# Kernel tuning notes

Measured on AMD Instinct MI355X. Metric: run time of the kernel, lower is better.

The kernel has to match this reference:

```python
import jax, jax.numpy as jnp
import numpy as np
import math

B, S, HID, H = 2, 1024, 768, 12
D = HID // H  # 64
ALPHA = 32.0


def setup_inputs() -> dict:
    key = jax.random.key(0)
    ks = jax.random.split(key, 8)
    return {
        "hidden_states": jax.random.normal(ks[0], (B, S, HID), jnp.float32),
        "attention_mask": jnp.zeros((B, 1, 1, S), jnp.float32),
        "head_mask": jnp.ones((1, H, 1, 1), jnp.float32),
        "rel_pos": jax.random.normal(ks[1], (B, H, S, S), jnp.float32),
        "rel_2d_pos": jax.random.normal(ks[2], (B, H, S, S), jnp.float32),
        "Wq": jax.random.normal(ks[3], (HID, HID), jnp.float32) * 0.02,
        "bq": jnp.zeros((HID,), jnp.float32),
        "Wk": jax.random.normal(ks[4], (HID, HID), jnp.float32) * 0.02,
        "bk": jnp.zeros((HID,), jnp.float32),
        "Wv": jax.random.normal(ks[5], (HID, HID), jnp.float32) * 0.02,
        "bv": jnp.zeros((HID,), jnp.float32),
    }


def _heads(x):
    # [B,S,HID] -> [B,H,S,D]
    return x.reshape(B, S, H, D).transpose(0, 2, 1, 3)


def cogview_softmax(scores, alpha=ALPHA):
    s = scores / alpha
    m = jnp.max(s, axis=-1, keepdims=True)
    return jax.nn.softmax((s - m) * alpha, axis=-1)


def reference(hidden_states, attention_mask, head_mask, rel_pos, rel_2d_pos,
              Wq, bq, Wk, bk, Wv, bv):
    norm = math.sqrt(D)
    q = _heads(hidden_states @ Wq + bq) / norm   # [B,H,S,D]
    k = _heads(hidden_states @ Wk + bk)
    v = _heads(hidden_states @ Wv + bv)
    scores = jnp.einsum("bhsd,bhtd->bhst", q, k)
    scores = scores + (rel_pos + rel_2d_pos) / norm
    scores = scores + attention_mask
    probs = cogview_softmax(scores)              # [B,H,S,S]
    probs = probs * head_mask
    ctx = jnp.einsum("bhst,bhtd->bhsd", probs, v)
    ctx = ctx.transpose(0, 2, 1, 3).reshape(B, S, HID)
    return ctx
```

## Files before the change

### kernel.cpp

```cpp
#include <hip/hip_runtime.h>
#include <hip/hip_bf16.h>
#include <cstdint>

#define BB   2
#define SS   1024
#define HIDD 768
#define NH   12
#define DH   64
#define BH   (BB*NH)

typedef short bf16x8 __attribute__((ext_vector_type(8)));
typedef float f32x4  __attribute__((ext_vector_type(4)));

__device__ __forceinline__ unsigned short f2b(float x) {
    union { float f; uint32_t u; } v; v.f = x;
    uint32_t u = v.u;
    uint32_t r = (u + 0x7fffu + ((u >> 16) & 1u)) >> 16;
    return (unsigned short)r;
}

__device__ __forceinline__ void async16(const void* g, void* l) {
    __builtin_amdgcn_global_load_lds(
        (const __attribute__((address_space(1))) unsigned int*)g,
        (__attribute__((address_space(3))) unsigned int*)l,
        16, 0, 0);
}

__global__ void cvt_x(const float* __restrict__ x, unsigned short* __restrict__ xb) {
    int i = blockIdx.x * blockDim.x + threadIdx.x;
    float4 v = ((const float4*)x)[i];
    ushort4 o;
    o.x = f2b(v.x); o.y = f2b(v.y); o.z = f2b(v.z); o.w = f2b(v.w);
    ((ushort4*)xb)[i] = o;
}

__global__ void transpose_w(const float* __restrict__ Wq, const float* __restrict__ Wk,
                            const float* __restrict__ Wv, unsigned short* __restrict__ Wt) {
    __shared__ float tile[32][33];
    const int w = blockIdx.z;
    const float* W = (w == 0) ? Wq : (w == 1) ? Wk : Wv;
    const int tx = threadIdx.x & 31, ty = threadIdx.x >> 5;
    const int k0 = blockIdx.x * 32, n0 = blockIdx.y * 32;
    for (int p = 0; p < 4; ++p)
        tile[ty + p * 8][tx] = W[(k0 + ty + p * 8) * HIDD + n0 + tx];
    __syncthreads();
    for (int p = 0; p < 4; ++p) {
        int n = n0 + ty + p * 8;
        Wt[(w * HIDD + n) * HIDD + k0 + tx] = f2b(tile[tx][ty + p * 8]);
    }
}

__global__ __launch_bounds__(256) void qkv_gemm(
    const unsigned short* __restrict__ Xb, const unsigned short* __restrict__ Wt,
    const float* __restrict__ bq, const float* __restrict__ bk, const float* __restrict__ bv,
    unsigned short* __restrict__ Qh, unsigned short* __restrict__ Kh,
    unsigned short* __restrict__ Vh) {
    __shared__ __align__(16) unsigned short lA[64 * 32];
    __shared__ __align__(16) unsigned short lB[128 * 32];
    const int t = threadIdx.x;
    const int wave = t >> 6, lane = t & 63;
    const int l15 = lane & 15, quad = lane >> 4;
    const int m0 = blockIdx.x * 64;
    const int n0 = blockIdx.y * 128;
    const int wm = (wave >> 1) * 32, wn = (wave & 1) * 64;

    f32x4 acc[2][4] = {};

    for (int k0 = 0; k0 < HIDD; k0 += 32) {
        __syncthreads();
        {
            int ldsA = (wave * 64) * 8;
            async16(Xb + (m0 + (t >> 2)) * HIDD + k0 + (t & 3) * 8, &lA[ldsA]);
            for (int r = 0; r < 2; ++r) {
                int i = r * 256 + t;
                int ldsB = (r * 256 + wave * 64) * 8;
                async16(Wt + (n0 + (i >> 2)) * HIDD + k0 + (i & 3) * 8, &lB[ldsB]);
            }
        }
        __syncthreads();

        bf16x8 af[2], bf[4];
        #pragma unroll
        for (int i = 0; i < 2; ++i)
            af[i] = *(const bf16x8*)&lA[(wm + i * 16 + l15) * 32 + quad * 8];
        #pragma unroll
        for (int j = 0; j < 4; ++j)
            bf[j] = *(const bf16x8*)&lB[(wn + j * 16 + l15) * 32 + quad * 8];
        #pragma unroll
        for (int i = 0; i < 2; ++i)
            #pragma unroll
            for (int j = 0; j < 4; ++j)
                acc[i][j] = __builtin_amdgcn_mfma_f32_16x16x32_bf16(af[i], bf[j], acc[i][j], 0, 0, 0);
    }

    const int sect = (n0 >= 1536) ? 2 : (n0 >= 768) ? 1 : 0;
    const float* bias = (sect == 0) ? bq : (sect == 1) ? bk : bv;
    unsigned short* dst = (sect == 0) ? Qh : (sect == 1) ? Kh : Vh;
    const float scale = (sect == 0) ? 0.125f : 1.0f;
    #pragma unroll
    for (int i = 0; i < 2; ++i) {
        #pragma unroll
        for (int j = 0; j < 4; ++j) {
            int n  = n0 + wn + j * 16 + l15;
            int nn = n - sect * HIDD;
            int h = nn >> 6, d = nn & 63;
            float bval = bias[nn];
            #pragma unroll
            for (int r = 0; r < 4; ++r) {
                int m = m0 + wm + i * 16 + quad * 4 + r;
                int b = m >> 10, s = m & 1023;
                float v = (acc[i][j][r] + bval) * scale;
                dst[((size_t)(b * NH + h) * SS + s) * DH + d] = f2b(v);
            }
        }
    }
}

__global__ __launch_bounds__(256) void transpose_v(
    const unsigned short* __restrict__ Vh, unsigned short* __restrict__ VhT) {
    __shared__ unsigned short tile[64][65];
    const int t = threadIdx.x;
    const int bh = blockIdx.y;
    const int s0 = blockIdx.x * 64;
    const int tx = t & 63, ty = t >> 6;
    const unsigned short* src = Vh + (size_t)bh * SS * DH;
    #pragma unroll
    for (int p = 0; p < 16; ++p)
        tile[ty + p * 4][tx] = src[(size_t)(s0 + ty + p * 4) * DH + tx];
    __syncthreads();
    unsigned short* dst = VhT + (size_t)bh * DH * SS;
    #pragma unroll
    for (int p = 0; p < 16; ++p)
        dst[(size_t)(ty + p * 4) * SS + s0 + tx] = tile[tx][ty + p * 4];
}

__global__ __launch_bounds__(256) void flash_attn(
    const unsigned short* __restrict__ Qh, const unsigned short* __restrict__ Kh,
    const unsigned short* __restrict__ VhT,
    const float* __restrict__ rel, const float* __restrict__ rel2d,
    const float* __restrict__ amask, const float* __restrict__ hmask,
    float* __restrict__ out) {
    __shared__ __align__(16) unsigned short Plds[4][16 * 72];
    __shared__ float o_lds[4][16][64];
    __shared__ float m_lds[4][16];
    __shared__ float l_lds[4][16];

    const int t = threadIdx.x;
    const int wave = t >> 6, lane = t & 63;
    const int l15 = lane & 15, quad = lane >> 4;
    const int bh = blockIdx.y;
    const int b = bh / NH, h = bh % NH;
    const int m0 = blockIdx.x * 16;

    const unsigned short* Qp = Qh + (size_t)bh * SS * DH;
    const unsigned short* Kp = Kh + (size_t)bh * SS * DH;
    const unsigned short* Vp = VhT + (size_t)bh * DH * SS;
    const float* relp  = rel   + (size_t)bh * SS * SS;
    const float* rel2p = rel2d + (size_t)bh * SS * SS;
    const float* maskp = amask + (size_t)b * SS;

    bf16x8 qf0 = *(const bf16x8*)&Qp[(m0 + l15) * DH + quad * 8];
    bf16x8 qf1 = *(const bf16x8*)&Qp[(m0 + l15) * DH + 32 + quad * 8];

    f32x4 o[4] = {};
    float mrow[4] = {-1e30f, -1e30f, -1e30f, -1e30f};
    float lrow[4] = {0.f, 0.f, 0.f, 0.f};
    unsigned short* Pw = &Plds[wave][0];

    const int jbeg = wave * 256, jend = jbeg + 256;
    for (int j0 = jbeg; j0 < jend; j0 += 64) {
        f32x4 sc[4] = {};
        #pragma unroll
        for (int c = 0; c < 4; ++c) {
            bf16x8 k0f = *(const bf16x8*)&Kp[(j0 + c * 16 + l15) * DH + quad * 8];
            bf16x8 k1f = *(const bf16x8*)&Kp[(j0 + c * 16 + l15) * DH + 32 + quad * 8];
            sc[c] = __builtin_amdgcn_mfma_f32_16x16x32_bf16(qf0, k0f, sc[c], 0, 0, 0);
            sc[c] = __builtin_amdgcn_mfma_f32_16x16x32_bf16(qf1, k1f, sc[c], 0, 0, 0);
        }
        float sv[4][4];
        #pragma unroll
        for (int c = 0; c < 4; ++c) {
            int col = j0 + c * 16 + l15;
            float mk = maskp[col];
            #pragma unroll
            for (int r = 0; r < 4; ++r) {
                size_t idx = (size_t)(m0 + quad * 4 + r) * SS + col;
                sv[c][r] = sc[c][r] + (relp[idx] + rel2p[idx]) * 0.125f + mk;
            }
        }
        float alpha[4];
        #pragma unroll
        for (int r = 0; r < 4; ++r) {
            float mx = fmaxf(fmaxf(sv[0][r], sv[1][r]), fmaxf(sv[2][r], sv[3][r]));
            #pragma unroll
            for (int off = 1; off < 16; off <<= 1) mx = fmaxf(mx, __shfl_xor(mx, off, 64));
            float mnew = fmaxf(mrow[r], mx);
            alpha[r] = __expf(mrow[r] - mnew);
            mrow[r] = mnew;
            float rs = 0.f;
            #pragma unroll
            for (int c = 0; c < 4; ++c) {
                float p = __expf(sv[c][r] - mnew);
                sv[c][r] = p;
                rs += p;
            }
            #pragma unroll
            for (int off = 1; off < 16; off <<= 1) rs += __shfl_xor(rs, off, 64);
            lrow[r] = lrow[r] * alpha[r] + rs;
            o[0][r] *= alpha[r]; o[1][r] *= alpha[r]; o[2][r] *= alpha[r]; o[3][r] *= alpha[r];
        }
        #pragma unroll
        for (int c = 0; c < 4; ++c)
            #pragma unroll
            for (int r = 0; r < 4; ++r)
                Pw[(quad * 4 + r) * 72 + c * 16 + l15] = f2b(sv[c][r]);

        bf16x8 pf0 = *(const bf16x8*)&Pw[l15 * 72 + quad * 8];
        bf16x8 pf1 = *(const bf16x8*)&Pw[l15 * 72 + 32 + quad * 8];
        #pragma unroll
        for (int dt = 0; dt < 4; ++dt) {
            bf16x8 v0 = *(const bf16x8*)&Vp[(dt * 16 + l15) * SS + j0 + quad * 8];
            bf16x8 v1 = *(const bf16x8*)&Vp[(dt * 16 + l15) * SS + j0 + 32 + quad * 8];
            o[dt] = __builtin_amdgcn_mfma_f32_16x16x32_bf16(pf0, v0, o[dt], 0, 0, 0);
            o[dt] = __builtin_amdgcn_mfma_f32_16x16x32_bf16(pf1, v1, o[dt], 0, 0, 0);
        }
    }

    #pragma unroll
    for (int dt = 0; dt < 4; ++dt)
        #pragma unroll
        for (int r = 0; r < 4; ++r)
            o_lds[wave][quad * 4 + r][dt * 16 + l15] = o[dt][r];
    if (l15 == 0) {
        #pragma unroll
        for (int r = 0; r < 4; ++r) {
            m_lds[wave][quad * 4 + r] = mrow[r];
            l_lds[wave][quad * 4 + r] = lrow[r];
        }
    }
    __syncthreads();

    const float hm = hmask[h];
    const int col = t & 63, rsel = t >> 6;
    #pragma unroll
    for (int rr = 0; rr < 4; ++rr) {
        int row = rsel * 4 + rr;
        float m01 = fmaxf(m_lds[0][row], m_lds[1][row]);
        float m23 = fmaxf(m_lds[2][row], m_lds[3][row]);
        float mt = fmaxf(m01, m23);
        float lt = 0.f, val = 0.f;
        #pragma unroll
        for (int w = 0; w < 4; ++w) {
            float sc = __expf(m_lds[w][row] - mt);
            lt += sc * l_lds[w][row];
            val += sc * o_lds[w][row][col];
        }
        int s = m0 + row;
        out[((size_t)(b * SS + s)) * HIDD + h * DH + col] = val * hm / lt;
    }
}

extern "C" void kernel_launch(void* const* d_in, const int* in_sizes, int n_in,
                              void* d_out, int out_size, void* d_ws, size_t ws_size,
                              hipStream_t stream) {
    const float* hs    = (const float*)d_in[0];
    const float* am    = (const float*)d_in[1];
    const float* hm    = (const float*)d_in[2];
    const float* rel   = (const float*)d_in[3];
    const float* rel2d = (const float*)d_in[4];
    const float* Wq    = (const float*)d_in[5];
    const float* bq    = (const float*)d_in[6];
    const float* Wk    = (const float*)d_in[7];
    const float* bk    = (const float*)d_in[8];
    const float* Wv    = (const float*)d_in[9];
    const float* bv    = (const float*)d_in[10];
    float* out = (float*)d_out;

    unsigned short* Xb  = (unsigned short*)d_ws;
    unsigned short* Wt  = Xb + 2048 * HIDD;
    unsigned short* Qh  = Wt + 3 * HIDD * HIDD;
    unsigned short* Kh  = Qh + (size_t)BH * SS * DH;
    unsigned short* Vh  = Kh + (size_t)BH * SS * DH;
    unsigned short* VhT = Vh + (size_t)BH * SS * DH;

    cvt_x<<<(2048 * HIDD / 4) / 256, 256, 0, stream>>>(hs, Xb);
    dim3 gT(24, 24, 3);
    transpose_w<<<gT, 256, 0, stream>>>(Wq, Wk, Wv, Wt);
    dim3 gG(32, 18);
    qkv_gemm<<<gG, 256, 0, stream>>>(Xb, Wt, bq, bk, bv, Qh, Kh, Vh);
    dim3 gV(16, BH);
    transpose_v<<<gV, 256, 0, stream>>>(Vh, VhT);
    dim3 gF(64, BH);
    flash_attn<<<gF, 256, 0, stream>>>(Qh, Kh, VhT, rel, rel2d, am, hm, out);
}
```

Before: 287.1 us.

## Vectorize rel-pos bias loads via LDS transpose and double-buffer QKV GEMM

In flash_attn, each lane now loads rel_pos, rel_2d_pos and the mask as float4 rows, so memory access is fully coalesced. The combined bias is then transposed through a per-wave LDS staging buffer into the MFMA accumulator layout, and that buffer is reused for the final cross-wave reduction. The QKV GEMM is retiled to 128x64 blocks with double-buffered async LDS loads, so the next k-slab is fetched while the current one is computed. The cost is extra LDS traffic for the staging step and one more barrier before the reduction.

Result: no change. 288.2 us (+0.4%).

```diff
diff --git a/kernel.cpp b/kernel.cpp
--- a/kernel.cpp
+++ b/kernel.cpp
@@ -55,37 +55,40 @@
     const float* __restrict__ bq, const float* __restrict__ bk, const float* __restrict__ bv,
     unsigned short* __restrict__ Qh, unsigned short* __restrict__ Kh,
     unsigned short* __restrict__ Vh) {
-    __shared__ __align__(16) unsigned short lA[64 * 32];
-    __shared__ __align__(16) unsigned short lB[128 * 32];
+    __shared__ __align__(16) unsigned short lA[2][128 * 32];
+    __shared__ __align__(16) unsigned short lB[2][64 * 32];
     const int t = threadIdx.x;
     const int wave = t >> 6, lane = t & 63;
     const int l15 = lane & 15, quad = lane >> 4;
-    const int m0 = blockIdx.x * 64;
-    const int n0 = blockIdx.y * 128;
-    const int wm = (wave >> 1) * 32, wn = (wave & 1) * 64;
+    const int m0 = blockIdx.x * 128;
+    const int n0 = blockIdx.y * 64;
+    const int wm = wave * 32;
 
     f32x4 acc[2][4] = {};
 
-    for (int k0 = 0; k0 < HIDD; k0 += 32) {
+    auto stage = [&](int k0, int b) {
+        #pragma unroll
+        for (int r = 0; r < 2; ++r) {
+            int ci = r * 256 + t;
+            async16(Xb + (m0 + (ci >> 2)) * HIDD + k0 + (ci & 3) * 8,
+                    &lA[b][(r * 256 + wave * 64) * 8]);
+        }
+        async16(Wt + (n0 + (t >> 2)) * HIDD + k0 + (t & 3) * 8,
+                &lB[b][(wave * 64) * 8]);
+    };
+
+    stage(0, 0);
+    for (int ki = 0; ki < 24; ++ki) {
+        const int cur = ki & 1;
         __syncthreads();
-        {
-            int ldsA = (wave * 64) * 8;
-            async16(Xb + (m0 + (t >> 2)) * HIDD + k0 + (t & 3) * 8, &lA[ldsA]);
-            for (int r = 0; r < 2; ++r) {
-                int i = r * 256 + t;
-                int ldsB = (r * 256 + wave * 64) * 8;
-                async16(Wt + (n0 + (i >> 2)) * HIDD + k0 + (i & 3) * 8, &lB[ldsB]);
-            }
-        }
-        __syncthreads();
-
+        if (ki < 23) stage((ki + 1) * 32, cur ^ 1);
         bf16x8 af[2], bf[4];
         #pragma unroll
         for (int i = 0; i < 2; ++i)
-            af[i] = *(const bf16x8*)&lA[(wm + i * 16 + l15) * 32 + quad * 8];
+            af[i] = *(const bf16x8*)&lA[cur][(wm + i * 16 + l15) * 32 + quad * 8];
         #pragma unroll
         for (int j = 0; j < 4; ++j)
-            bf[j] = *(const bf16x8*)&lB[(wn + j * 16 + l15) * 32 + quad * 8];
+            bf[j] = *(const bf16x8*)&lB[cur][(j * 16 + l15) * 32 + quad * 8];
         #pragma unroll
         for (int i = 0; i < 2; ++i)
             #pragma unroll
@@ -101,7 +104,7 @@
     for (int i = 0; i < 2; ++i) {
         #pragma unroll
         for (int j = 0; j < 4; ++j) {
-            int n  = n0 + wn + j * 16 + l15;
+            int n  = n0 + j * 16 + l15;
             int nn = n - sect * HIDD;
             int h = nn >> 6, d = nn & 63;
             float bval = bias[nn];
@@ -141,9 +144,7 @@
     const float* __restrict__ amask, const float* __restrict__ hmask,
     float* __restrict__ out) {
     __shared__ __align__(16) unsigned short Plds[4][16 * 72];
-    __shared__ float o_lds[4][16][64];
-    __shared__ float m_lds[4][16];
-    __shared__ float l_lds[4][16];
+    __shared__ __align__(16) float smem[5376];
 
     const int t = threadIdx.x;
     const int wave = t >> 6, lane = t & 63;
@@ -166,9 +167,19 @@
     float mrow[4] = {-1e30f, -1e30f, -1e30f, -1e30f};
     float lrow[4] = {0.f, 0.f, 0.f, 0.f};
     unsigned short* Pw = &Plds[wave][0];
+    float* stg = &smem[wave * 1344];
 
     const int jbeg = wave * 256, jend = jbeg + 256;
     for (int j0 = jbeg; j0 < jend; j0 += 64) {
+        f32x4 ra[4], rb[4];
+        #pragma unroll
+        for (int i = 0; i < 4; ++i) {
+            size_t base = (size_t)(m0 + 4 * i + quad) * SS + j0 + 4 * l15;
+            ra[i] = *(const f32x4*)&relp[base];
+            rb[i] = *(const f32x4*)&rel2p[base];
+        }
+        f32x4 mk4 = *(const f32x4*)&maskp[j0 + 4 * l15];
+
         f32x4 sc[4] = {};
         #pragma unroll
         for (int c = 0; c < 4; ++c) {
@@ -177,17 +188,21 @@
             sc[c] = __builtin_amdgcn_mfma_f32_16x16x32_bf16(qf0, k0f, sc[c], 0, 0, 0);
             sc[c] = __builtin_amdgcn_mfma_f32_16x16x32_bf16(qf1, k1f, sc[c], 0, 0, 0);
         }
+
+        #pragma unroll
+        for (int i = 0; i < 4; ++i)
+            #pragma unroll
+            for (int cc = 0; cc < 4; ++cc)
+                stg[(4 * l15 + cc) * 21 + 4 * i + quad] =
+                    (ra[i][cc] + rb[i][cc]) * 0.125f + mk4[cc];
+
         float sv[4][4];
         #pragma unroll
-        for (int c = 0; c < 4; ++c) {
-            int col = j0 + c * 16 + l15;
-            float mk = maskp[col];
-            #pragma unroll
-            for (int r = 0; r < 4; ++r) {
-                size_t idx = (size_t)(m0 + quad * 4 + r) * SS + col;
-                sv[c][r] = sc[c][r] + (relp[idx] + rel2p[idx]) * 0.125f + mk;
-            }
-        }
+        for (int c = 0; c < 4; ++c)
+            #pragma unroll
+            for (int r = 0; r < 4; ++r)
+                sv[c][r] = sc[c][r] + stg[(c * 16 + l15) * 21 + quad * 4 + r];
+
         float alpha[4];
         #pragma unroll
         for (int r = 0; r < 4; ++r) {
@@ -226,16 +241,20 @@
         }
     }
 
+    __syncthreads();
+    float* o_l = smem;
+    float* m_l = smem + 4096;
+    float* l_l = smem + 4160;
     #pragma unroll
     for (int dt = 0; dt < 4; ++dt)
         #pragma unroll
         for (int r = 0; r < 4; ++r)
-            o_lds[wave][quad * 4 + r][dt * 16 + l15] = o[dt][r];
+            o_l[(wave * 16 + quad * 4 + r) * 64 + dt * 16 + l15] = o[dt][r];
     if (l15 == 0) {
         #pragma unroll
         for (int r = 0; r < 4; ++r) {
-            m_lds[wave][quad * 4 + r] = mrow[r];
-            l_lds[wave][quad * 4 + r] = lrow[r];
+            m_l[wave * 16 + quad * 4 + r] = mrow[r];
+            l_l[wave * 16 + quad * 4 + r] = lrow[r];
         }
     }
     __syncthreads();
@@ -245,15 +264,15 @@
     #pragma unroll
     for (int rr = 0; rr < 4; ++rr) {
         int row = rsel * 4 + rr;
-        float m01 = fmaxf(m_lds[0][row], m_lds[1][row]);
-        float m23 = fmaxf(m_lds[2][row], m_lds[3][row]);
+        float m01 = fmaxf(m_l[row], m_l[16 + row]);
+        float m23 = fmaxf(m_l[32 + row], m_l[48 + row]);
         float mt = fmaxf(m01, m23);
         float lt = 0.f, val = 0.f;
         #pragma unroll
         for (int w = 0; w < 4; ++w) {
-            float sc = __expf(m_lds[w][row] - mt);
-            lt += sc * l_lds[w][row];
-            val += sc * o_lds[w][row][col];
+            float sc = __expf(m_l[w * 16 + row] - mt);
+            lt += sc * l_l[w * 16 + row];
+            val += sc * o_l[(w * 16 + row) * 64 + col];
         }
         int s = m0 + row;
         out[((size_t)(b * SS + s)) * HIDD + h * DH + col] = val * hm / lt;
@@ -286,7 +305,7 @@
     cvt_x<<<(2048 * HIDD / 4) / 256, 256, 0, stream>>>(hs, Xb);
     dim3 gT(24, 24, 3);
     transpose_w<<<gT, 256, 0, stream>>>(Wq, Wk, Wv, Wt);
-    dim3 gG(32, 18);
+    dim3 gG(16, 36);
     qkv_gemm<<<gG, 256, 0, stream>>>(Xb, Wt, bq, bk, bv, Qh, Kh, Vh);
     dim3 gV(16, BH);
     transpose_v<<<gV, 256, 0, stream>>>(Vh, VhT);
```
